# Kernel tuning notes

Measured on AMD Instinct MI355X. Metric: run time of the kernel, lower is better.

## Reference

```python
import jax, jax.numpy as jnp
import numpy as np

B, L, H, D, VOC, C, P = 16, 256, 6, 768, 32000, 20, 1
d = D // H
MAXF = 20
BN_EPS = 1e-5


def setup_inputs() -> dict:
    key = jax.random.key(0)
    ks = jax.random.split(key, 8)
    doc_tids = jax.random.randint(ks[0], (B, L), 0, VOC)
    TFs = jax.random.uniform(ks[1], (B, L), dtype=jnp.float32) * 20.0 + 1.0
    DFs = jax.random.uniform(ks[2], (B, L), dtype=jnp.float32) * 1000.0 + 1.0
    emb = jax.random.normal(ks[3], (VOC, D), dtype=jnp.float32) * 0.02
    fcW = jax.random.normal(ks[4], (C + P, D), dtype=jnp.float32) * 0.02
    fcb = jnp.zeros((C + P,), dtype=jnp.float32)
    weiW = jax.random.normal(ks[5], (2, H), dtype=jnp.float32) * 0.1
    weib = jnp.zeros((2,), dtype=jnp.float32)
    return dict(doc_tids=doc_tids, TFs=TFs, DFs=DFs, emb=emb,
                fcW=fcW, fcb=fcb, weiW=weiW, weib=weib)


def _bn(x):
    # BatchNorm over channel axis 1 (H), batch stats over all other axes (train mode, affine=False)
    m = x.mean(axis=(0, 2, 3), keepdims=True)
    v = x.var(axis=(0, 2, 3), keepdims=True)
    return (x - m) * jax.lax.rsqrt(v + BN_EPS)


def _leaky9(x):
    return jnp.where(x >= 0, x, 9.0 * x)


def reference(doc_tids, TFs, DFs, emb, fcW, fcb, weiW, weib):
    # --- EmbbedingTFIDF (eval mode, dropout off): tf-idf weighted embedding lookup ---
    tf = jnp.minimum(TFs, float(MAXF))
    idf = jnp.log1p(1.0 / DFs)
    x = emb[doc_tids] * (tf * idf)[:, :, None]          # (B, L, D)
    valid = doc_tids != 0
    # model flips pad_mask with logical_not, then co_weights[pad_mask] = 0
    invalid = ~(valid[:, :, None] & valid[:, None, :])  # (B, L, L) True -> zero out
    mask = invalid[:, None, :, :]                       # broadcast over heads

    def split_heads(h):
        return h.reshape(B, L, H, d).transpose(0, 2, 1, 3)  # (B, H, L, d)

    Q = split_heads(x)
    K = Q
    V = Q

    # --- nearAttention (layers=1) ---
    Vn = _bn(V)
    # DistMatrix: pairwise Euclidean distance dist[b,h,i,j] = ||K_i - Q_j||
    Ksq = jnp.sum(K * K, axis=-1)[..., :, None]
    Qsq = jnp.sum(Q * Q, axis=-1)[..., None, :]
    cross = jnp.einsum('bhid,bhjd->bhij', K, Q)
    co = jnp.sqrt(jnp.maximum(Ksq + Qsq - 2.0 * cross, 1e-12))  # (B, H, L, L)
    # BatchNorm1d(H) over flattened (B, H, L*L) == per-H stats over (0,2,3)
    co = _leaky9(_bn(co))
    co = jnp.where(mask, 0.0, co)
    co = jax.nn.softmax(co, axis=-1)
    co = jnp.where(jnp.isnan(co), 0.0, co)
    V_out = jnp.einsum('bhij,bhjd->bhid', co, Vn)
    Q_out = _bn(jnp.einsum('bhij,bhjd->bhid', co, Q))
    K_out = _bn(jnp.einsum('bhij,bhjd->bhid', co, K))

    # --- head ---
    Vc = V_out.transpose(0, 2, 1, 3).reshape(B, L, D)       # catHiddens
    V_lgts = jax.nn.softmax(Vc @ fcW.T + fcb, axis=-1)      # (B, L, C+P)
    cw = jnp.swapaxes(co, -1, -2).reshape(B, L * L, H)      # transpose then contiguous reshape
    cw = jax.nn.softmax(cw @ weiW.T + weib, axis=-1)        # (B, L*L, 2)
    cw = cw.reshape(B, L, L, 2).sum(axis=-2, keepdims=True)[:, :, :, 0]  # (B, L, 1)
    cw = jax.nn.softmax(cw, axis=-1)                        # softmax over singleton -> ones (faithful)
    logits = (cw * V_lgts).sum(axis=1)[:, :C]               # (B, C)
    logits = jax.nn.softmax(logits, axis=-1)
    return logits
```

## Files before the change

### kernel.cpp

```cpp
#include <hip/hip_runtime.h>
#include <hip/hip_bf16.h>
#include <math.h>

#define Bb 16
#define Ll 256
#define Hh 6
#define Dm 768
#define dh 128

#define OFF_VC   0UL
#define OFF_SQ   0UL
#define OFF_THS  24576UL
#define OFF_PART 49152UL
#define OFF_CO   3145728UL
#define OFF_XH   9437184UL
#define OFF_XT   11010048UL
#define OFF_STAT 12582912UL
#define OFF_ACC  12582936UL

typedef __attribute__((ext_vector_type(8))) __bf16 bf16x8;
typedef __attribute__((ext_vector_type(4))) float f32x4;

__global__ __launch_bounds__(128) void k1_gather(const int* __restrict__ tids,
    const float* __restrict__ TF, const float* __restrict__ DF,
    const float* __restrict__ emb, __hip_bfloat16* __restrict__ xh,
    float* __restrict__ sq, float* __restrict__ ths) {
  int tok = blockIdx.x;
  int t = threadIdx.x;
  int tid = tids[tok];
  float w = fminf(TF[tok], 20.0f) * log1pf(1.0f / DF[tok]);
  const float* er = emb + (size_t)tid * Dm;
  int bb = tok >> 8, l = tok & 255;
  float v[6];
#pragma unroll
  for (int k = 0; k < 6; ++k) {
    float e = er[t + 128 * k] * w;
    __hip_bfloat16 hb = __float2bfloat16(e);
    float f = __bfloat162float(hb);
    xh[(((size_t)(bb * 6 + k)) * 256 + l) * 128 + t] = hb;
    v[k] = f;
  }
  __shared__ float s1[6][2], s2[6][2];
  int lane = t & 63, wid = t >> 6;
#pragma unroll
  for (int k = 0; k < 6; ++k) {
    float a = v[k], q = v[k] * v[k];
#pragma unroll
    for (int off = 32; off >= 1; off >>= 1) {
      a += __shfl_down(a, off);
      q += __shfl_down(q, off);
    }
    if (lane == 0) { s1[k][wid] = a; s2[k][wid] = q; }
  }
  __syncthreads();
  if (t < 6) {
    size_t idx = ((size_t)(bb * 6 + t)) * 256 + l;
    ths[idx] = s1[t][0] + s1[t][1];
    sq[idx]  = s2[t][0] + s2[t][1];
  }
}

__global__ __launch_bounds__(256) void k1t_transpose(const __hip_bfloat16* __restrict__ xh,
    __hip_bfloat16* __restrict__ xT) {
  int tb = blockIdx.x;
  int bh = blockIdx.y;
  int T0 = tb * 64;
  __shared__ __hip_bfloat16 tile[64][130];
  int tid = threadIdx.x;
  {
    int r = tid >> 2, cg = tid & 3;
    const __hip_bfloat16* src = xh + ((size_t)(bh * 256 + T0 + r)) * 128 + cg * 32;
#pragma unroll
    for (int j4 = 0; j4 < 4; ++j4) {
      const unsigned int* s32 = (const unsigned int*)(src + j4 * 8);
#pragma unroll
      for (int u = 0; u < 4; ++u)
        *(unsigned int*)&tile[r][cg * 32 + j4 * 8 + 2 * u] = s32[u];
    }
  }
  __syncthreads();
  int tp = tid & 31, c0 = tid >> 5;
  unsigned int* xT32 = (unsigned int*)xT;
#pragma unroll
  for (int i = 0; i < 16; ++i) {
    int c = i * 8 + c0;
    unsigned int lo = *(const unsigned short*)&tile[2 * tp][c];
    unsigned int hi = *(const unsigned short*)&tile[2 * tp + 1][c];
    xT32[((size_t)(bh * 128 + c)) * 128 + T0 / 2 + tp] = lo | (hi << 16);
  }
}

__global__ __launch_bounds__(256) void k2_dist(const __hip_bfloat16* __restrict__ xh,
    const float* __restrict__ sq, float* __restrict__ co, float* __restrict__ part) {
  int bh = blockIdx.y;
  int p = blockIdx.x;
  int rb = p >> 1, cb = p & 1;
  int tid = threadIdx.x, w = tid >> 6, lane = tid & 63;
  int quad = lane >> 4, l16 = lane & 15;
  int I = rb * 64 + w * 16;
  int J = cb * 128;
  const __bf16* xb = (const __bf16*)(xh) + (size_t)bh * 256 * 128;
  bf16x8 a[4];
#pragma unroll
  for (int k0 = 0; k0 < 4; ++k0)
    a[k0] = *(const bf16x8*)(xb + (size_t)(I + l16) * 128 + k0 * 32 + quad * 8);
  const float* sqh = sq + (size_t)bh * 256;
  float si[4];
#pragma unroll
  for (int r = 0; r < 4; ++r) si[r] = sqh[I + quad * 4 + r];
  float* cob = co + (size_t)bh * 256 * 256;
  float ls1 = 0.0f, ls2 = 0.0f;
#pragma unroll
  for (int jt = 0; jt < 8; ++jt) {
    int Jc = J + jt * 16;
    f32x4 acc = {0.0f, 0.0f, 0.0f, 0.0f};
#pragma unroll
    for (int k0 = 0; k0 < 4; ++k0) {
      bf16x8 bfr = *(const bf16x8*)(xb + (size_t)(Jc + l16) * 128 + k0 * 32 + quad * 8);
      acc = __builtin_amdgcn_mfma_f32_16x16x32_bf16(a[k0], bfr, acc, 0, 0, 0);
    }
    float sj = sqh[Jc + l16];
#pragma unroll
    for (int r = 0; r < 4; ++r) {
      float d2 = si[r] + sj - 2.0f * acc[r];
      float cv = sqrtf(fmaxf(d2, 1e-12f));
      cob[(size_t)(I + quad * 4 + r) * 256 + (Jc + l16)] = cv;
      ls1 += cv; ls2 += cv * cv;
    }
  }
#pragma unroll
  for (int off = 32; off >= 1; off >>= 1) {
    ls1 += __shfl_down(ls1, off);
    ls2 += __shfl_down(ls2, off);
  }
  __shared__ float rs[2][4];
  if (lane == 0) { rs[0][w] = ls1; rs[1][w] = ls2; }
  __syncthreads();
  if (tid == 0) {
    part[((size_t)bh * 8 + p) * 2 + 0] = rs[0][0] + rs[0][1] + rs[0][2] + rs[0][3];
    part[((size_t)bh * 8 + p) * 2 + 1] = rs[1][0] + rs[1][1] + rs[1][2] + rs[1][3];
  }
}

__global__ __launch_bounds__(384) void k3_stats(const float* __restrict__ ths,
    const float* __restrict__ sq, const float* __restrict__ part,
    float* __restrict__ stats, float* __restrict__ acc) {
  int h = threadIdx.x >> 6, lane = threadIdx.x & 63;
  float s1 = 0.0f, s2 = 0.0f;
  for (int m = 0; m < 64; ++m) {
    int f = m * 64 + lane;
    int bb = f >> 8, l = f & 255;
    size_t idx = ((size_t)(bb * 6 + h)) * 256 + l;
    s1 += ths[idx]; s2 += sq[idx];
  }
#pragma unroll
  for (int off = 32; off >= 1; off >>= 1) {
    s1 += __shfl_down(s1, off);
    s2 += __shfl_down(s2, off);
  }
  if (lane == 0) {
    float cnt = 524288.0f;
    float mean = s1 / cnt;
    float var = s2 / cnt - mean * mean;
    stats[h] = mean;
    stats[6 + h] = rsqrtf(var + 1e-5f);
  }
  float c1 = 0.0f, c2 = 0.0f;
#pragma unroll
  for (int t = 0; t < 2; ++t) {
    int e = lane + 64 * t;
    int bb = e >> 3, pp = e & 7;
    size_t pidx = ((size_t)(bb * 6 + h) * 8 + pp) * 2;
    c1 += part[pidx]; c2 += part[pidx + 1];
  }
#pragma unroll
  for (int off = 32; off >= 1; off >>= 1) {
    c1 += __shfl_down(c1, off);
    c2 += __shfl_down(c2, off);
  }
  if (lane == 0) {
    float cnt = 1048576.0f;
    float mean = c1 / cnt;
    float var = c2 / cnt - mean * mean;
    stats[12 + h] = mean;
    stats[18 + h] = rsqrtf(var + 1e-5f);
  }
  if (threadIdx.x < 336) acc[threadIdx.x] = 0.0f;
}

__global__ __launch_bounds__(256) void k4_softmax(float* __restrict__ co,
    const int* __restrict__ tids, const float* __restrict__ stats) {
  int row = blockIdx.x * 4 + (threadIdx.x >> 6);
  int lane = threadIdx.x & 63;
  int bh = row >> 8, i = row & 255;
  int b = bh / 6, h = bh % 6;
  float m = stats[12 + h], r = stats[18 + h];
  float* cr = co + (size_t)row * 256;
  float4 v = *(float4*)(cr + lane * 4);
  float t0 = (v.x - m) * r, t1 = (v.y - m) * r, t2 = (v.z - m) * r, t3 = (v.w - m) * r;
  t0 = t0 >= 0.0f ? t0 : 9.0f * t0;
  t1 = t1 >= 0.0f ? t1 : 9.0f * t1;
  t2 = t2 >= 0.0f ? t2 : 9.0f * t2;
  t3 = t3 >= 0.0f ? t3 : 9.0f * t3;
  const int* tb = tids + b * 256;
  int vi = (tb[i] != 0);
  int4 tj = *(const int4*)(tb + lane * 4);
  if (!vi || tj.x == 0) t0 = 0.0f;
  if (!vi || tj.y == 0) t1 = 0.0f;
  if (!vi || tj.z == 0) t2 = 0.0f;
  if (!vi || tj.w == 0) t3 = 0.0f;
  float mx = fmaxf(fmaxf(t0, t1), fmaxf(t2, t3));
#pragma unroll
  for (int off = 32; off >= 1; off >>= 1) mx = fmaxf(mx, __shfl_xor(mx, off));
  float e0 = expf(t0 - mx), e1 = expf(t1 - mx), e2 = expf(t2 - mx), e3 = expf(t3 - mx);
  float s = e0 + e1 + e2 + e3;
#pragma unroll
  for (int off = 32; off >= 1; off >>= 1) s += __shfl_xor(s, off);
  float inv = 1.0f / s;
  ushort4 pk;
  pk.x = __bfloat16_as_ushort(__float2bfloat16(e0 * inv));
  pk.y = __bfloat16_as_ushort(__float2bfloat16(e1 * inv));
  pk.z = __bfloat16_as_ushort(__float2bfloat16(e2 * inv));
  pk.w = __bfloat16_as_ushort(__float2bfloat16(e3 * inv));
  *(ushort4*)((__hip_bfloat16*)cr + lane * 4) = pk;
}

__global__ __launch_bounds__(256) void k5a_vout(const __hip_bfloat16* __restrict__ co_bf,
    const __hip_bfloat16* __restrict__ xT, const float* __restrict__ stats,
    float* __restrict__ vc) {
  int it = blockIdx.x;
  int bh = blockIdx.y;
  int b = bh / 6, h = bh % 6;
  int tid = threadIdx.x, w = tid >> 6, lane = tid & 63;
  int quad = lane >> 4, l16 = lane & 15;
  int I = it * 64 + w * 16;
  const __bf16* cb = (const __bf16*)co_bf + ((size_t)(bh * 256 + I + l16)) * 512;
  bf16x8 a[8];
#pragma unroll
  for (int k0 = 0; k0 < 8; ++k0)
    a[k0] = *(const bf16x8*)(cb + k0 * 32 + quad * 8);
  const __bf16* xb = (const __bf16*)xT + (size_t)bh * 128 * 256;
  float m = stats[h], rs = stats[6 + h];
  float rm = rs * m;
  float* vcb = vc + ((size_t)(b * 256 + I + quad * 4)) * 768 + h * 128;
#pragma unroll
  for (int jt = 0; jt < 8; ++jt) {
    int ch = jt * 16 + l16;
    const __bf16* brow = xb + (size_t)ch * 256;
    f32x4 acc = {0.0f, 0.0f, 0.0f, 0.0f};
#pragma unroll
    for (int k0 = 0; k0 < 8; ++k0) {
      bf16x8 bfr = *(const bf16x8*)(brow + k0 * 32 + quad * 8);
      acc = __builtin_amdgcn_mfma_f32_16x16x32_bf16(a[k0], bfr, acc, 0, 0, 0);
    }
#pragma unroll
    for (int r = 0; r < 4; ++r)
      vcb[(size_t)r * 768 + ch] = rs * acc[r] - rm;
  }
}

__global__ __launch_bounds__(256) void k5b_lgts(const float* __restrict__ vc,
    const float* __restrict__ fcW, const float* __restrict__ fcb,
    float* __restrict__ acc) {
  int wid = threadIdx.x >> 6, lane = threadIdx.x & 63;
  int token = blockIdx.x * 4 + wid;
  int b = token >> 8;
  const float* vr = vc + (size_t)token * Dm;
  float part[21];
#pragma unroll
  for (int c = 0; c < 21; ++c) part[c] = 0.0f;
  for (int m = 0; m < 12; ++m) {
    float v = vr[lane + 64 * m];
#pragma unroll
    for (int c = 0; c < 21; ++c)
      part[c] += v * fcW[c * 768 + lane + 64 * m];
  }
#pragma unroll
  for (int c = 0; c < 21; ++c) {
#pragma unroll
    for (int off = 32; off >= 1; off >>= 1)
      part[c] += __shfl_down(part[c], off);
  }
  __shared__ float sp[4][21];
  if (lane == 0) {
    float mx = -1e30f;
#pragma unroll
    for (int c = 0; c < 21; ++c) { part[c] += fcb[c]; mx = fmaxf(mx, part[c]); }
    float s = 0.0f;
#pragma unroll
    for (int c = 0; c < 21; ++c) { part[c] = expf(part[c] - mx); s += part[c]; }
    float inv = 1.0f / s;
#pragma unroll
    for (int c = 0; c < 21; ++c) sp[wid][c] = part[c] * inv;
  }
  __syncthreads();
  if (threadIdx.x < 21) {
    float s = sp[0][threadIdx.x] + sp[1][threadIdx.x] + sp[2][threadIdx.x] + sp[3][threadIdx.x];
    atomicAdd(&acc[b * 21 + threadIdx.x], s);
  }
}

__global__ __launch_bounds__(64) void k6_final(const float* __restrict__ acc,
                                               float* __restrict__ out) {
  int b = threadIdx.x;
  if (b < 16) {
    float mx = -1e30f;
    for (int c = 0; c < 20; ++c) mx = fmaxf(mx, acc[b * 21 + c]);
    float e[20], s = 0.0f;
    for (int c = 0; c < 20; ++c) { e[c] = expf(acc[b * 21 + c] - mx); s += e[c]; }
    float inv = 1.0f / s;
    for (int c = 0; c < 20; ++c) out[b * 20 + c] = e[c] * inv;
  }
}

extern "C" void kernel_launch(void* const* d_in, const int* in_sizes, int n_in,
                              void* d_out, int out_size, void* d_ws, size_t ws_size,
                              hipStream_t stream) {
  const int*   tids = (const int*)d_in[0];
  const float* TF   = (const float*)d_in[1];
  const float* DF   = (const float*)d_in[2];
  const float* emb  = (const float*)d_in[3];
  const float* fcW  = (const float*)d_in[4];
  const float* fcb  = (const float*)d_in[5];
  float* out = (float*)d_out;
  float* ws  = (float*)d_ws;
  float* vc    = ws + OFF_VC;
  float* sq    = ws + OFF_SQ;
  float* ths   = ws + OFF_THS;
  float* part  = ws + OFF_PART;
  float* co    = ws + OFF_CO;
  __hip_bfloat16* xh = (__hip_bfloat16*)(ws + OFF_XH);
  __hip_bfloat16* xT = (__hip_bfloat16*)(ws + OFF_XT);
  float* stats = ws + OFF_STAT;
  float* acc   = ws + OFF_ACC;

  k1_gather<<<4096, 128, 0, stream>>>(tids, TF, DF, emb, xh, sq, ths);
  k1t_transpose<<<dim3(4, 96), 256, 0, stream>>>(xh, xT);
  k2_dist<<<dim3(8, 96), 256, 0, stream>>>(xh, sq, co, part);
  k3_stats<<<1, 384, 0, stream>>>(ths, sq, part, stats, acc);
  k4_softmax<<<6144, 256, 0, stream>>>(co, tids, stats);
  k5a_vout<<<dim3(4, 96), 256, 0, stream>>>((const __hip_bfloat16*)co, xT, stats, vc);
  k5b_lgts<<<1024, 256, 0, stream>>>(vc, fcW, fcb, acc);
  k6_final<<<1, 64, 0, stream>>>(acc, out);
}
```

Measured before the change: 223.5 us.

## Recompute distances in fused softmax, merge gather+transpose, MFMA logits head

```diff
diff --git a/kernel.cpp b/kernel.cpp
--- a/kernel.cpp
+++ b/kernel.cpp
@@ -2,104 +2,85 @@
 #include <hip/hip_bf16.h>
 #include <math.h>
 
-#define Bb 16
-#define Ll 256
-#define Hh 6
-#define Dm 768
-#define dh 128
-
-#define OFF_VC   0UL
-#define OFF_SQ   0UL
-#define OFF_THS  24576UL
-#define OFF_PART 49152UL
+#define OFF_XH   0UL
+#define OFF_XT   1572864UL
 #define OFF_CO   3145728UL
-#define OFF_XH   9437184UL
-#define OFF_XT   11010048UL
-#define OFF_STAT 12582912UL
-#define OFF_ACC  12582936UL
+#define OFF_VC   6291456UL
+#define OFF_SQ   7864320UL
+#define OFF_THS  7888896UL
+#define OFF_PART 7913472UL
+#define OFF_STAT 7914240UL
+#define OFF_ACC  7914264UL
 
 typedef __attribute__((ext_vector_type(8))) __bf16 bf16x8;
 typedef __attribute__((ext_vector_type(4))) float f32x4;
-
-__global__ __launch_bounds__(128) void k1_gather(const int* __restrict__ tids,
+typedef __attribute__((ext_vector_type(8))) unsigned short u16x8;
+
+__global__ __launch_bounds__(256) void k1_gather(const int* __restrict__ tids,
     const float* __restrict__ TF, const float* __restrict__ DF,
-    const float* __restrict__ emb, __hip_bfloat16* __restrict__ xh,
-    float* __restrict__ sq, float* __restrict__ ths) {
-  int tok = blockIdx.x;
-  int t = threadIdx.x;
-  int tid = tids[tok];
-  float w = fminf(TF[tok], 20.0f) * log1pf(1.0f / DF[tok]);
-  const float* er = emb + (size_t)tid * Dm;
-  int bb = tok >> 8, l = tok & 255;
-  float v[6];
-#pragma unroll
-  for (int k = 0; k < 6; ++k) {
-    float e = er[t + 128 * k] * w;
-    __hip_bfloat16 hb = __float2bfloat16(e);
-    float f = __bfloat162float(hb);
-    xh[(((size_t)(bb * 6 + k)) * 256 + l) * 128 + t] = hb;
-    v[k] = f;
-  }
-  __shared__ float s1[6][2], s2[6][2];
-  int lane = t & 63, wid = t >> 6;
-#pragma unroll
-  for (int k = 0; k < 6; ++k) {
-    float a = v[k], q = v[k] * v[k];
-#pragma unroll
-    for (int off = 32; off >= 1; off >>= 1) {
-      a += __shfl_down(a, off);
-      q += __shfl_down(q, off);
-    }
-    if (lane == 0) { s1[k][wid] = a; s2[k][wid] = q; }
+    const float* __restrict__ emb, unsigned short* __restrict__ xh,
+    unsigned short* __restrict__ xT, float* __restrict__ sq, float* __restrict__ ths) {
+  int bh = blockIdx.x >> 2, tg = blockIdx.x & 3;
+  int b = bh / 6, h = bh % 6;
+  int T0 = tg * 64;
+  int tid = threadIdx.x;
+  __shared__ float swgt[64];
+  __shared__ int stid[64];
+  __shared__ unsigned short tT[128][66];
+  if (tid < 64) {
+    int tok = b * 256 + T0 + tid;
+    stid[tid] = tids[tok];
+    swgt[tid] = fminf(TF[tok], 20.0f) * log1pf(1.0f / DF[tok]);
   }
   __syncthreads();
-  if (t < 6) {
-    size_t idx = ((size_t)(bb * 6 + t)) * 256 + l;
-    ths[idx] = s1[t][0] + s1[t][1];
-    sq[idx]  = s2[t][0] + s2[t][1];
-  }
-}
-
-__global__ __launch_bounds__(256) void k1t_transpose(const __hip_bfloat16* __restrict__ xh,
-    __hip_bfloat16* __restrict__ xT) {
-  int tb = blockIdx.x;
-  int bh = blockIdx.y;
-  int T0 = tb * 64;
-  __shared__ __hip_bfloat16 tile[64][130];
-  int tid = threadIdx.x;
-  {
-    int r = tid >> 2, cg = tid & 3;
-    const __hip_bfloat16* src = xh + ((size_t)(bh * 256 + T0 + r)) * 128 + cg * 32;
-#pragma unroll
-    for (int j4 = 0; j4 < 4; ++j4) {
-      const unsigned int* s32 = (const unsigned int*)(src + j4 * 8);
-#pragma unroll
-      for (int u = 0; u < 4; ++u)
-        *(unsigned int*)&tile[r][cg * 32 + j4 * 8 + 2 * u] = s32[u];
-    }
-  }
+  int r = tid >> 2, cq = (tid & 3) * 32;
+  const float* er = emb + (size_t)stid[r] * 768 + h * 128 + cq;
+  float wgt = swgt[r];
+  float s1 = 0.0f, s2 = 0.0f;
+  unsigned short v16[32];
+#pragma unroll
+  for (int j4 = 0; j4 < 8; ++j4) {
+    float4 e4 = *(const float4*)(er + j4 * 4);
+    float f[4] = {e4.x * wgt, e4.y * wgt, e4.z * wgt, e4.w * wgt};
+#pragma unroll
+    for (int e = 0; e < 4; ++e) {
+      __hip_bfloat16 hb = __float2bfloat16(f[e]);
+      float g = __bfloat162float(hb);
+      s1 += g; s2 += g * g;
+      v16[j4 * 4 + e] = __bfloat16_as_ushort(hb);
+    }
+  }
+  unsigned short* xr = xh + ((size_t)(bh * 256 + T0 + r)) * 128 + cq;
+#pragma unroll
+  for (int g = 0; g < 4; ++g) {
+    u16x8 pk;
+#pragma unroll
+    for (int e = 0; e < 8; ++e) pk[e] = v16[g * 8 + e];
+    *(u16x8*)(xr + g * 8) = pk;
+  }
+  s1 += __shfl_down(s1, 1); s1 += __shfl_down(s1, 2);
+  s2 += __shfl_down(s2, 1); s2 += __shfl_down(s2, 2);
+  if ((tid & 3) == 0) {
+    ths[bh * 256 + T0 + r] = s1;
+    sq[bh * 256 + T0 + r]  = s2;
+  }
+#pragma unroll
+  for (int j = 0; j < 32; ++j) tT[cq + j][r] = v16[j];
   __syncthreads();
-  int tp = tid & 31, c0 = tid >> 5;
-  unsigned int* xT32 = (unsigned int*)xT;
-#pragma unroll
-  for (int i = 0; i < 16; ++i) {
-    int c = i * 8 + c0;
-    unsigned int lo = *(const unsigned short*)&tile[2 * tp][c];
-    unsigned int hi = *(const unsigned short*)&tile[2 * tp + 1][c];
-    xT32[((size_t)(bh * 128 + c)) * 128 + T0 / 2 + tp] = lo | (hi << 16);
-  }
-}
-
-__global__ __launch_bounds__(256) void k2_dist(const __hip_bfloat16* __restrict__ xh,
-    const float* __restrict__ sq, float* __restrict__ co, float* __restrict__ part) {
-  int bh = blockIdx.y;
-  int p = blockIdx.x;
-  int rb = p >> 1, cb = p & 1;
+  int c = tid >> 1, half = tid & 1;
+  const unsigned int* row32 = (const unsigned int*)&tT[c][0];
+  unsigned int* xo = (unsigned int*)(xT) + ((size_t)(bh * 128 + c)) * 128 + tg * 32 + half * 16;
+#pragma unroll
+  for (int k = 0; k < 16; ++k) xo[k] = row32[half * 16 + k];
+}
+
+__global__ __launch_bounds__(256) void k2_stats(const unsigned short* __restrict__ xh,
+    const float* __restrict__ sq, float* __restrict__ part) {
+  int p = blockIdx.x, bh = blockIdx.y;
   int tid = threadIdx.x, w = tid >> 6, lane = tid & 63;
   int quad = lane >> 4, l16 = lane & 15;
-  int I = rb * 64 + w * 16;
-  int J = cb * 128;
-  const __bf16* xb = (const __bf16*)(xh) + (size_t)bh * 256 * 128;
+  int I = p * 64 + w * 16;
+  const __bf16* xb = (const __bf16*)xh + (size_t)bh * 256 * 128;
   bf16x8 a[4];
 #pragma unroll
   for (int k0 = 0; k0 < 4; ++k0)
@@ -108,23 +89,19 @@
   float si[4];
 #pragma unroll
   for (int r = 0; r < 4; ++r) si[r] = sqh[I + quad * 4 + r];
-  float* cob = co + (size_t)bh * 256 * 256;
   float ls1 = 0.0f, ls2 = 0.0f;
 #pragma unroll
-  for (int jt = 0; jt < 8; ++jt) {
-    int Jc = J + jt * 16;
+  for (int t = 0; t < 16; ++t) {
     f32x4 acc = {0.0f, 0.0f, 0.0f, 0.0f};
 #pragma unroll
     for (int k0 = 0; k0 < 4; ++k0) {
-      bf16x8 bfr = *(const bf16x8*)(xb + (size_t)(Jc + l16) * 128 + k0 * 32 + quad * 8);
+      bf16x8 bfr = *(const bf16x8*)(xb + (size_t)(t * 16 + l16) * 128 + k0 * 32 + quad * 8);
       acc = __builtin_amdgcn_mfma_f32_16x16x32_bf16(a[k0], bfr, acc, 0, 0, 0);
     }
-    float sj = sqh[Jc + l16];
+    float sj = sqh[t * 16 + l16];
 #pragma unroll
     for (int r = 0; r < 4; ++r) {
-      float d2 = si[r] + sj - 2.0f * acc[r];
-      float cv = sqrtf(fmaxf(d2, 1e-12f));
-      cob[(size_t)(I + quad * 4 + r) * 256 + (Jc + l16)] = cv;
+      float cv = sqrtf(fmaxf(si[r] + sj - 2.0f * acc[r], 1e-12f));
       ls1 += cv; ls2 += cv * cv;
     }
   }
@@ -137,8 +114,8 @@
   if (lane == 0) { rs[0][w] = ls1; rs[1][w] = ls2; }
   __syncthreads();
   if (tid == 0) {
-    part[((size_t)bh * 8 + p) * 2 + 0] = rs[0][0] + rs[0][1] + rs[0][2] + rs[0][3];
-    part[((size_t)bh * 8 + p) * 2 + 1] = rs[1][0] + rs[1][1] + rs[1][2] + rs[1][3];
+    part[((size_t)bh * 4 + p) * 2 + 0] = rs[0][0] + rs[0][1] + rs[0][2] + rs[0][3];
+    part[((size_t)bh * 4 + p) * 2 + 1] = rs[1][0] + rs[1][1] + rs[1][2] + rs[1][3];
   }
 }
 
@@ -165,14 +142,9 @@
     stats[h] = mean;
     stats[6 + h] = rsqrtf(var + 1e-5f);
   }
-  float c1 = 0.0f, c2 = 0.0f;
-#pragma unroll
-  for (int t = 0; t < 2; ++t) {
-    int e = lane + 64 * t;
-    int bb = e >> 3, pp = e & 7;
-    size_t pidx = ((size_t)(bb * 6 + h) * 8 + pp) * 2;
-    c1 += part[pidx]; c2 += part[pidx + 1];
-  }
+  int bb2 = lane >> 2, pp = lane & 3;
+  size_t pidx = ((size_t)(bb2 * 6 + h) * 4 + pp) * 2;
+  float c1 = part[pidx], c2 = part[pidx + 1];
 #pragma unroll
   for (int off = 32; off >= 1; off >>= 1) {
     c1 += __shfl_down(c1, off);
@@ -188,53 +160,84 @@
   if (threadIdx.x < 336) acc[threadIdx.x] = 0.0f;
 }
 
-__global__ __launch_bounds__(256) void k4_softmax(float* __restrict__ co,
-    const int* __restrict__ tids, const float* __restrict__ stats) {
-  int row = blockIdx.x * 4 + (threadIdx.x >> 6);
-  int lane = threadIdx.x & 63;
-  int bh = row >> 8, i = row & 255;
+__global__ __launch_bounds__(256) void k4_fused(const unsigned short* __restrict__ xh,
+    const int* __restrict__ tids, const float* __restrict__ sq,
+    const float* __restrict__ stats, unsigned short* __restrict__ co16) {
+  int p = blockIdx.x, bh = blockIdx.y;
   int b = bh / 6, h = bh % 6;
-  float m = stats[12 + h], r = stats[18 + h];
-  float* cr = co + (size_t)row * 256;
-  float4 v = *(float4*)(cr + lane * 4);
-  float t0 = (v.x - m) * r, t1 = (v.y - m) * r, t2 = (v.z - m) * r, t3 = (v.w - m) * r;
-  t0 = t0 >= 0.0f ? t0 : 9.0f * t0;
-  t1 = t1 >= 0.0f ? t1 : 9.0f * t1;
-  t2 = t2 >= 0.0f ? t2 : 9.0f * t2;
-  t3 = t3 >= 0.0f ? t3 : 9.0f * t3;
-  const int* tb = tids + b * 256;
-  int vi = (tb[i] != 0);
-  int4 tj = *(const int4*)(tb + lane * 4);
-  if (!vi || tj.x == 0) t0 = 0.0f;
-  if (!vi || tj.y == 0) t1 = 0.0f;
-  if (!vi || tj.z == 0) t2 = 0.0f;
-  if (!vi || tj.w == 0) t3 = 0.0f;
-  float mx = fmaxf(fmaxf(t0, t1), fmaxf(t2, t3));
-#pragma unroll
-  for (int off = 32; off >= 1; off >>= 1) mx = fmaxf(mx, __shfl_xor(mx, off));
-  float e0 = expf(t0 - mx), e1 = expf(t1 - mx), e2 = expf(t2 - mx), e3 = expf(t3 - mx);
-  float s = e0 + e1 + e2 + e3;
-#pragma unroll
-  for (int off = 32; off >= 1; off >>= 1) s += __shfl_xor(s, off);
-  float inv = 1.0f / s;
-  ushort4 pk;
-  pk.x = __bfloat16_as_ushort(__float2bfloat16(e0 * inv));
-  pk.y = __bfloat16_as_ushort(__float2bfloat16(e1 * inv));
-  pk.z = __bfloat16_as_ushort(__float2bfloat16(e2 * inv));
-  pk.w = __bfloat16_as_ushort(__float2bfloat16(e3 * inv));
-  *(ushort4*)((__hip_bfloat16*)cr + lane * 4) = pk;
-}
-
-__global__ __launch_bounds__(256) void k5a_vout(const __hip_bfloat16* __restrict__ co_bf,
-    const __hip_bfloat16* __restrict__ xT, const float* __restrict__ stats,
-    float* __restrict__ vc) {
+  int tid = threadIdx.x, w = tid >> 6, lane = tid & 63;
+  int quad = lane >> 4, l16 = lane & 15;
+  int I = p * 64 + w * 16;
+  __shared__ float svld[256];
+  __shared__ float ssq[256];
+  svld[tid] = (tids[b * 256 + tid] != 0) ? 1.0f : 0.0f;
+  ssq[tid] = sq[(size_t)bh * 256 + tid];
+  const __bf16* xb = (const __bf16*)xh + (size_t)bh * 256 * 128;
+  bf16x8 a[4];
+#pragma unroll
+  for (int k0 = 0; k0 < 4; ++k0)
+    a[k0] = *(const bf16x8*)(xb + (size_t)(I + l16) * 128 + k0 * 32 + quad * 8);
+  __syncthreads();
+  float m = stats[12 + h], rsc = stats[18 + h];
+  float rv[4], si[4];
+#pragma unroll
+  for (int r = 0; r < 4; ++r) {
+    rv[r] = svld[I + quad * 4 + r];
+    si[r] = ssq[I + quad * 4 + r];
+  }
+  float y[16][4];
+#pragma unroll
+  for (int t = 0; t < 16; ++t) {
+    f32x4 acc = {0.0f, 0.0f, 0.0f, 0.0f};
+#pragma unroll
+    for (int k0 = 0; k0 < 4; ++k0) {
+      bf16x8 bfr = *(const bf16x8*)(xb + (size_t)(t * 16 + l16) * 128 + k0 * 32 + quad * 8);
+      acc = __builtin_amdgcn_mfma_f32_16x16x32_bf16(a[k0], bfr, acc, 0, 0, 0);
+    }
+    float sj = ssq[t * 16 + l16];
+    float cvld = svld[t * 16 + l16];
+#pragma unroll
+    for (int r = 0; r < 4; ++r) {
+      float cv = sqrtf(fmaxf(si[r] + sj - 2.0f * acc[r], 1e-12f));
+      float yv = (cv - m) * rsc;
+      yv = yv >= 0.0f ? yv : 9.0f * yv;
+      y[t][r] = yv * rv[r] * cvld;
+    }
+  }
+  float inv[4];
+#pragma unroll
+  for (int r = 0; r < 4; ++r) {
+    float mx = y[0][r];
+#pragma unroll
+    for (int t = 1; t < 16; ++t) mx = fmaxf(mx, y[t][r]);
+#pragma unroll
+    for (int off = 1; off <= 8; off <<= 1) mx = fmaxf(mx, __shfl_xor(mx, off));
+    float s = 0.0f;
+#pragma unroll
+    for (int t = 0; t < 16; ++t) { y[t][r] = expf(y[t][r] - mx); s += y[t][r]; }
+#pragma unroll
+    for (int off = 1; off <= 8; off <<= 1) s += __shfl_xor(s, off);
+    inv[r] = 1.0f / s;
+  }
+  size_t rowbase = ((size_t)bh * 256 + I + quad * 4) * 256;
+#pragma unroll
+  for (int t = 0; t < 16; ++t)
+#pragma unroll
+    for (int r = 0; r < 4; ++r)
+      co16[rowbase + (size_t)r * 256 + t * 16 + l16] =
+          __bfloat16_as_ushort(__float2bfloat16(y[t][r] * inv[r]));
+}
+
+__global__ __launch_bounds__(256) void k5a_vout(const unsigned short* __restrict__ co16,
+    const unsigned short* __restrict__ xT, const float* __restrict__ stats,
+    unsigned short* __restrict__ vc16) {
   int it = blockIdx.x;
   int bh = blockIdx.y;
   int b = bh / 6, h = bh % 6;
   int tid = threadIdx.x, w = tid >> 6, lane = tid & 63;
   int quad = lane >> 4, l16 = lane & 15;
   int I = it * 64 + w * 16;
-  const __bf16* cb = (const __bf16*)co_bf + ((size_t)(bh * 256 + I + l16)) * 512;
+  const __bf16* cb = (const __bf16*)co16 + ((size_t)(bh * 256 + I + l16)) * 256;
   bf16x8 a[8];
 #pragma unroll
   for (int k0 = 0; k0 < 8; ++k0)
@@ -242,7 +245,7 @@
   const __bf16* xb = (const __bf16*)xT + (size_t)bh * 128 * 256;
   float m = stats[h], rs = stats[6 + h];
   float rm = rs * m;
-  float* vcb = vc + ((size_t)(b * 256 + I + quad * 4)) * 768 + h * 128;
+  size_t vbase = ((size_t)(b * 256 + I + quad * 4)) * 768 + h * 128;
 #pragma unroll
   for (int jt = 0; jt < 8; ++jt) {
     int ch = jt * 16 + l16;
@@ -254,50 +257,60 @@
       acc = __builtin_amdgcn_mfma_f32_16x16x32_bf16(a[k0], bfr, acc, 0, 0, 0);
     }
 #pragma unroll
-    for (int r = 0; r < 4; ++r)
-      vcb[(size_t)r * 768 + ch] = rs * acc[r] - rm;
-  }
-}
-
-__global__ __launch_bounds__(256) void k5b_lgts(const float* __restrict__ vc,
+    for (int r = 0; r < 4; ++r) {
+      float ov = rs * acc[r] - rm;
+      vc16[vbase + (size_t)r * 768 + ch] = __bfloat16_as_ushort(__float2bfloat16(ov));
+    }
+  }
+}
+
+__global__ __launch_bounds__(256) void k5b_lgts(const unsigned short* __restrict__ vc16,
     const float* __restrict__ fcW, const float* __restrict__ fcb,
     float* __restrict__ acc) {
-  int wid = threadIdx.x >> 6, lane = threadIdx.x & 63;
-  int token = blockIdx.x * 4 + wid;
-  int b = token >> 8;
-  const float* vr = vc + (size_t)token * Dm;
-  float part[21];
-#pragma unroll
-  for (int c = 0; c < 21; ++c) part[c] = 0.0f;
-  for (int m = 0; m < 12; ++m) {
-    float v = vr[lane + 64 * m];
-#pragma unroll
-    for (int c = 0; c < 21; ++c)
-      part[c] += v * fcW[c * 768 + lane + 64 * m];
-  }
-#pragma unroll
-  for (int c = 0; c < 21; ++c) {
-#pragma unroll
-    for (int off = 32; off >= 1; off >>= 1)
-      part[c] += __shfl_down(part[c], off);
-  }
-  __shared__ float sp[4][21];
-  if (lane == 0) {
-    float mx = -1e30f;
-#pragma unroll
-    for (int c = 0; c < 21; ++c) { part[c] += fcb[c]; mx = fmaxf(mx, part[c]); }
-    float s = 0.0f;
-#pragma unroll
-    for (int c = 0; c < 21; ++c) { part[c] = expf(part[c] - mx); s += part[c]; }
+  int tid = threadIdx.x, w = tid >> 6, lane = tid & 63;
+  int quad = lane >> 4, l16 = lane & 15;
+  int tok0 = blockIdx.x * 64 + w * 16;
+  int b = blockIdx.x >> 2;
+  int c1c = (l16 < 5) ? (16 + l16) : 20;
+  const __bf16* vb = (const __bf16*)vc16;
+  const float* w0 = fcW + (size_t)l16 * 768;
+  const float* w1 = fcW + (size_t)c1c * 768;
+  f32x4 ac0 = {0.0f, 0.0f, 0.0f, 0.0f}, ac1 = {0.0f, 0.0f, 0.0f, 0.0f};
+#pragma unroll
+  for (int k0 = 0; k0 < 24; ++k0) {
+    int ko = k0 * 32 + quad * 8;
+    bf16x8 af = *(const bf16x8*)(vb + (size_t)(tok0 + l16) * 768 + ko);
+    bf16x8 b0, b1;
+#pragma unroll
+    for (int e = 0; e < 8; ++e) {
+      b0[e] = (__bf16)w0[ko + e];
+      b1[e] = (__bf16)w1[ko + e];
+    }
+    ac0 = __builtin_amdgcn_mfma_f32_16x16x32_bf16(af, b0, ac0, 0, 0, 0);
+    ac1 = __builtin_amdgcn_mfma_f32_16x16x32_bf16(af, b1, ac1, 0, 0, 0);
+  }
+  float bias0 = fcb[l16];
+  float bias1 = (l16 < 5) ? fcb[16 + l16] : 0.0f;
+  float p0s = 0.0f, p1s = 0.0f;
+#pragma unroll
+  for (int r = 0; r < 4; ++r) {
+    float lg0 = ac0[r] + bias0;
+    float lg1 = (l16 < 5) ? (ac1[r] + bias1) : -1e30f;
+    float mx = fmaxf(lg0, lg1);
+#pragma unroll
+    for (int off = 1; off <= 8; off <<= 1) mx = fmaxf(mx, __shfl_xor(mx, off));
+    float e0 = expf(lg0 - mx), e1 = expf(lg1 - mx);
+    float s = e0 + e1;
+#pragma unroll
+    for (int off = 1; off <= 8; off <<= 1) s += __shfl_xor(s, off);
     float inv = 1.0f / s;
-#pragma unroll
-    for (int c = 0; c < 21; ++c) sp[wid][c] = part[c] * inv;
-  }
-  __syncthreads();
-  if (threadIdx.x < 21) {
-    float s = sp[0][threadIdx.x] + sp[1][threadIdx.x] + sp[2][threadIdx.x] + sp[3][threadIdx.x];
-    atomicAdd(&acc[b * 21 + threadIdx.x], s);
-  }
+    p0s += e0 * inv;
+    p1s += e1 * inv;
+  }
+  p0s += __shfl_xor(p0s, 16); p0s += __shfl_xor(p0s, 32);
+  p1s += __shfl_xor(p1s, 16); p1s += __shfl_xor(p1s, 32);
+  if (quad == 0) atomicAdd(&acc[b * 21 + l16], p0s);
+  if (quad == 1 && l16 < 5) atomicAdd(&acc[b * 21 + 16 + l16], p1s);
 }
 
 __global__ __launch_bounds__(64) void k6_final(const float* __restrict__ acc,
@@ -324,22 +337,21 @@
   const float* fcb  = (const float*)d_in[5];
   float* out = (float*)d_out;
   float* ws  = (float*)d_ws;
-  float* vc    = ws + OFF_VC;
+  unsigned short* xh = (unsigned short*)(ws + OFF_XH);
+  unsigned short* xT = (unsigned short*)(ws + OFF_XT);
+  unsigned short* co = (unsigned short*)(ws + OFF_CO);
+  unsigned short* vc = (unsigned short*)(ws + OFF_VC);
   float* sq    = ws + OFF_SQ;
   float* ths   = ws + OFF_THS;
   float* part  = ws + OFF_PART;
-  float* co    = ws + OFF_CO;
-  __hip_bfloat16* xh = (__hip_bfloat16*)(ws + OFF_XH);
-  __hip_bfloat16* xT = (__hip_bfloat16*)(ws + OFF_XT);
   float* stats = ws + OFF_STAT;
   float* acc   = ws + OFF_ACC;
 
-  k1_gather<<<4096, 128, 0, stream>>>(tids, TF, DF, emb, xh, sq, ths);
-  k1t_transpose<<<dim3(4, 96), 256, 0, stream>>>(xh, xT);
-  k2_dist<<<dim3(8, 96), 256, 0, stream>>>(xh, sq, co, part);
+  k1_gather<<<384, 256, 0, stream>>>(tids, TF, DF, emb, xh, xT, sq, ths);
+  k2_stats<<<dim3(4, 96), 256, 0, stream>>>(xh, sq, part);
   k3_stats<<<1, 384, 0, stream>>>(ths, sq, part, stats, acc);
-  k4_softmax<<<6144, 256, 0, stream>>>(co, tids, stats);
-  k5a_vout<<<dim3(4, 96), 256, 0, stream>>>((const __hip_bfloat16*)co, xT, stats, vc);
-  k5b_lgts<<<1024, 256, 0, stream>>>(vc, fcW, fcb, acc);
+  k4_fused<<<dim3(4, 96), 256, 0, stream>>>(xh, tids, sq, stats, co);
+  k5a_vout<<<dim3(4, 96), 256, 0, stream>>>(co, xT, stats, vc);
+  k5b_lgts<<<64, 256, 0, stream>>>(vc, fcW, fcb, acc);
   k6_final<<<1, 64, 0, stream>>>(acc, out);
 }
```

New measurement: 235.8 us. 1.06x slower.
